# Kernel optimization log

Hardware: AMD Instinct MI355X
Metric: run time of the kernel (lower is better)

The kernel has to match this reference:

```python
import jax, jax.numpy as jnp
import numpy as np

# ---- module hyperparameters (from init_kwargs) ----
R, C = 16, 16            # layer.rows, layer.cols
STRIDE = 0               # layer.stride (shared receptive field)
KH = KW = 8              # layer.kernel_size
CIN, COUT = 16, 64       # in/out channels
T = 7                    # spike time steps (== maxweight)
MAXW = 7.0
UCAPTURE, UMINUS, USEARCH, UBACKOFF, UMIN = 0.102, 0.051, 0.032, 0.96, 0.008


def setup_inputs() -> dict:
    key = jax.random.key(0)
    k1, k2, k3 = jax.random.split(key, 3)
    input_spikes = jax.random.randint(k1, (T, CIN, KH, KW), 0, 2).astype(jnp.int32)
    output_spikes = jax.random.randint(k2, (T, COUT, R, C), 0, 2).astype(jnp.int32)
    # integer-valued weights in [0, maxweight], stored as float for the update math
    weight = jax.random.randint(k3, (R, C, COUT, CIN, KH, KW), 0, int(MAXW) + 1).astype(jnp.float32)
    return {"weight": weight, "input_spikes": input_spikes, "output_spikes": output_spikes}


def reference(weight, input_spikes, output_spikes):
    # spike-time codes: fewer spikes -> later time
    x_times = int(MAXW) - jnp.sum(input_spikes, axis=0)    # [CIN, KH, KW] (H==KH, W==KW)
    y_times = int(MAXW) - jnp.sum(output_spikes, axis=0)   # [COUT, R, C]

    # gather the receptive-field patch for every (row, col) column (static indices)
    rr = (np.arange(R) * STRIDE)[:, None] + np.arange(KH)  # [R, KH]
    cc = (np.arange(C) * STRIDE)[:, None] + np.arange(KW)  # [C, KW]
    # advanced indexing -> [CIN, R, C, KH, KW]
    x_patch = x_times[:, rr[:, None, :, None], cc[None, :, None, :]]
    bx = jnp.transpose(x_patch, (1, 2, 0, 3, 4))[:, :, None, :, :, :]   # [R,C,1,CIN,KH,KW]
    by = jnp.transpose(y_times, (1, 2, 0))[:, :, :, None, None, None]   # [R,C,COUT,1,1,1]

    A = bx == int(MAXW)
    B = by == int(MAXW)
    Cgt = bx > by

    zero = jnp.float32(0.0)
    probs_plus = jnp.where(~A & B, USEARCH, jnp.where(~A & ~B & ~Cgt, UCAPTURE, zero))
    probs_minus = jnp.where(A & ~B, UBACKOFF, jnp.where(~A & ~B & Cgt, UMINUS, zero))
    # broadcast to full weight shape
    shape = weight.shape
    probs_plus = jnp.broadcast_to(probs_plus, shape)
    probs_minus = jnp.broadcast_to(probs_minus, shape)

    key = jax.random.key(42)
    k1, k2, k3, k4, k5 = jax.random.split(key, 5)
    dt = weight.dtype
    bern_plus = (jax.random.uniform(k1, shape) < probs_plus)
    bern_minus = (jax.random.uniform(k2, shape) < probs_minus)

    ratio = weight * (1.0 / MAXW)
    F_minus_raw = jax.random.uniform(k3, shape) < (1.0 - ratio) * (1.0 + ratio)
    F_plus_raw = jax.random.uniform(k4, shape) < ratio * (2.0 - ratio)
    umin_bern = jax.random.uniform(k5, shape) < UMIN
    # torch.max of two {0,1} frames == logical OR
    F_plus = jnp.logical_or(F_plus_raw, umin_bern).astype(dt)
    F_minus = jnp.logical_or(F_minus_raw, umin_bern).astype(dt)

    new_w = weight + bern_plus.astype(dt) * F_plus - bern_minus.astype(dt) * F_minus
    new_w = jnp.clip(new_w, 0.0, MAXW)  # integer-valued floats, cast to int in torch
    return new_w
```

## Files before the change

### kernel.cpp

```cpp
#include <hip/hip_runtime.h>
#include <stdint.h>


#define N_TOTAL 16777216
#define Y_SIZE 16384
#define X_SIZE 1024

struct U2 { uint32_t a, b; };

constexpr uint32_t rotl_c(uint32_t x, int r) {
  return (x << r) | (x >> (32 - r));
}

constexpr U2 threefry_c(uint32_t k0, uint32_t k1, uint32_t x0, uint32_t x1) {
  uint32_t ks2 = k0 ^ k1 ^ 0x1BD11BDAu;
  x0 += k0; x1 += k1;
  x0 += x1; x1 = rotl_c(x1, 13); x1 ^= x0;
  x0 += x1; x1 = rotl_c(x1, 15); x1 ^= x0;
  x0 += x1; x1 = rotl_c(x1, 26); x1 ^= x0;
  x0 += x1; x1 = rotl_c(x1, 6);  x1 ^= x0;
  x0 += k1; x1 += ks2 + 1u;
  x0 += x1; x1 = rotl_c(x1, 17); x1 ^= x0;
  x0 += x1; x1 = rotl_c(x1, 29); x1 ^= x0;
  x0 += x1; x1 = rotl_c(x1, 16); x1 ^= x0;
  x0 += x1; x1 = rotl_c(x1, 24); x1 ^= x0;
  x0 += ks2; x1 += k0 + 2u;
  x0 += x1; x1 = rotl_c(x1, 13); x1 ^= x0;
  x0 += x1; x1 = rotl_c(x1, 15); x1 ^= x0;
  x0 += x1; x1 = rotl_c(x1, 26); x1 ^= x0;
  x0 += x1; x1 = rotl_c(x1, 6);  x1 ^= x0;
  x0 += k0; x1 += k1 + 3u;
  x0 += x1; x1 = rotl_c(x1, 17); x1 ^= x0;
  x0 += x1; x1 = rotl_c(x1, 29); x1 ^= x0;
  x0 += x1; x1 = rotl_c(x1, 16); x1 ^= x0;
  x0 += x1; x1 = rotl_c(x1, 24); x1 ^= x0;
  x0 += k1; x1 += ks2 + 4u;
  x0 += x1; x1 = rotl_c(x1, 13); x1 ^= x0;
  x0 += x1; x1 = rotl_c(x1, 15); x1 ^= x0;
  x0 += x1; x1 = rotl_c(x1, 26); x1 ^= x0;
  x0 += x1; x1 = rotl_c(x1, 6);  x1 ^= x0;
  x0 += ks2; x1 += k0 + 5u;
  return {x0, x1};
}

constexpr U2 SK1 = threefry_c(0u, 42u, 0u, 0u);
constexpr U2 SK2 = threefry_c(0u, 42u, 0u, 1u);
constexpr U2 SK3 = threefry_c(0u, 42u, 0u, 2u);
constexpr U2 SK4 = threefry_c(0u, 42u, 0u, 3u);
constexpr U2 SK5 = threefry_c(0u, 42u, 0u, 4u);

constexpr uint32_t KS2_3 = SK3.a ^ SK3.b ^ 0x1BD11BDAu;
constexpr uint32_t KS2_4 = SK4.a ^ SK4.b ^ 0x1BD11BDAu;
constexpr uint32_t KS2_5 = SK5.a ^ SK5.b ^ 0x1BD11BDAu;

constexpr uint32_t bern_thr(float pf) {
  double p8 = (double)pf * 8388608.0;
  uint64_t t = (uint64_t)p8;
  if ((double)t < p8) t += 1u;
  return (uint32_t)(t << 9);
}
constexpr uint32_t T_SEARCH  = bern_thr(0.032f);
constexpr uint32_t T_CAPTURE = bern_thr(0.102f);
constexpr uint32_t T_BACKOFF = bern_thr(0.96f);
constexpr uint32_t T_MINUS   = bern_thr(0.051f);
constexpr uint32_t T_UMIN    = bern_thr(0.008f);

__device__ __forceinline__ uint32_t rotl_d(uint32_t x, int r) {
  return __builtin_amdgcn_alignbit(x, x, 32 - r);
}

__device__ __forceinline__ uint32_t tf_fold_k(uint32_t k0, uint32_t k1,
                                              uint32_t ks2, uint32_t ctr) {
  uint32_t x0 = k0;
  uint32_t x1 = ctr + k1;
  x0 += x1; x1 = rotl_d(x1, 13); x1 ^= x0;
  x0 += x1; x1 = rotl_d(x1, 15); x1 ^= x0;
  x0 += x1; x1 = rotl_d(x1, 26); x1 ^= x0;
  x0 += x1; x1 = rotl_d(x1, 6);  x1 ^= x0;
  x0 += k1; x1 += ks2 + 1u;
  x0 += x1; x1 = rotl_d(x1, 17); x1 ^= x0;
  x0 += x1; x1 = rotl_d(x1, 29); x1 ^= x0;
  x0 += x1; x1 = rotl_d(x1, 16); x1 ^= x0;
  x0 += x1; x1 = rotl_d(x1, 24); x1 ^= x0;
  x0 += ks2; x1 += k0 + 2u;
  x0 += x1; x1 = rotl_d(x1, 13); x1 ^= x0;
  x0 += x1; x1 = rotl_d(x1, 15); x1 ^= x0;
  x0 += x1; x1 = rotl_d(x1, 26); x1 ^= x0;
  x0 += x1; x1 = rotl_d(x1, 6);  x1 ^= x0;
  x0 += k0; x1 += k1 + 3u;
  x0 += x1; x1 = rotl_d(x1, 17); x1 ^= x0;
  x0 += x1; x1 = rotl_d(x1, 29); x1 ^= x0;
  x0 += x1; x1 = rotl_d(x1, 16); x1 ^= x0;
  x0 += x1; x1 = rotl_d(x1, 24); x1 ^= x0;
  x0 += k1; x1 += ks2 + 4u;
  x0 += x1; x1 = rotl_d(x1, 13); x1 ^= x0;
  x0 += x1; x1 = rotl_d(x1, 15); x1 ^= x0;
  x0 += x1; x1 = rotl_d(x1, 26); x1 ^= x0;
  x0 += x1; x1 = rotl_d(x1, 6);  x1 ^= x0;
  x0 += ks2; x1 += k0 + 5u;
  return x0 ^ x1;
}

__device__ __forceinline__ float bits_to_unit_float(uint32_t bits) {
  uint32_t fb = (bits >> 9) | 0x3f800000u;
  return __uint_as_float(fb) - 1.0f;
}

__device__ __forceinline__ uint32_t mbcnt64(uint64_t m) {
  return __builtin_amdgcn_mbcnt_hi((uint32_t)(m >> 32),
         __builtin_amdgcn_mbcnt_lo((uint32_t)m, 0u));
}

__global__ void precompute_times(const int* __restrict__ in_sp,
                                 const int* __restrict__ out_sp,
                                 int* __restrict__ xt, int* __restrict__ yt) {
  int tid = blockIdx.x * 256 + threadIdx.x;
  if (tid < Y_SIZE) {
    int s = 0;
#pragma unroll
    for (int t = 0; t < 7; ++t) s += out_sp[t * Y_SIZE + tid];
    yt[tid] = 7 - s;
  } else if (tid < Y_SIZE + X_SIZE) {
    int j = tid - Y_SIZE;
    int s = 0;
#pragma unroll
    for (int t = 0; t < 7; ++t) s += in_sp[t * X_SIZE + j];
    xt[j] = 7 - s;
  }
}

__global__ __launch_bounds__(256) void modstdp4t(const float* __restrict__ w,
                                                 const int* __restrict__ xt,
                                                 const int* __restrict__ yt,
                                                 float* __restrict__ out) {
  __shared__ uint4 tbl[64];
  __shared__ uint2 rec[1024];
  __shared__ uint32_t okb[1024];

  uint32_t tid = threadIdx.x;

  if (tid < 64u) {
    uint32_t bx = tid >> 3, by = tid & 7u;
    bool A = (bx == 7u), B = (by == 7u), Cg = (bx > by);
    uint32_t thr = A ? (B ? 0u : T_BACKOFF)
                     : (B ? T_SEARCH : (Cg ? T_MINUS : T_CAPTURE));
    bool selM = A ? !B : (!B && Cg);
    uint32_t k0 = selM ? SK2.a : SK1.a;
    uint32_t k1 = selM ? SK2.b : SK1.b;
    tbl[tid] = make_uint4(thr | (uint32_t)selM, k0, k1,
                          k0 ^ k1 ^ 0x1BD11BDAu);
  }
  __syncthreads();

  uint32_t lane = tid & 63u;
  uint32_t wbase = (tid >> 6) * 256u;
  uint32_t t = blockIdx.x * 256u + tid;
  uint32_t i0 = t * 4u;

  float4 wv = *reinterpret_cast<const float4*>(w + i0);
  int4 bxv = *reinterpret_cast<const int4*>(xt + (i0 & 1023u));
  float warr[4]; *reinterpret_cast<float4*>(warr) = wv;
  int barr[4];   *reinterpret_cast<int4*>(barr) = bxv;

  uint32_t cout = (i0 >> 10) & 63u;
  uint32_t c = (i0 >> 16) & 15u;
  uint32_t r = i0 >> 20;
  uint32_t by = (uint32_t)yt[cout * 256u + r * 16u + c];

  bool hit[4];
  uint32_t sMb[4];
  uint32_t rank[4];
  uint32_t cnt = 0;

#pragma unroll
  for (int e = 0; e < 4; ++e) {
    uint32_t i = i0 + (uint32_t)e;
    uint4 en = tbl[(uint32_t)barr[e] * 8u + by];
    uint32_t thr = en.x & 0xFFFFFE00u;
    uint32_t selMb = en.x & 1u;
    sMb[e] = selMb;

    uint32_t bits12 = tf_fold_k(en.y, en.z, en.w, i);
    bool h = bits12 < thr;
    hit[e] = h;

    uint64_t m = __ballot(h);
    cnt += (uint32_t)__popcll(m);
    if (h) {
      uint32_t rk = (cnt - (uint32_t)__popcll(m)) + mbcnt64(m);
      rank[e] = rk;
      rec[wbase + rk] = make_uint2(i | (selMb << 31),
                                   __float_as_uint(warr[e]));
    }
  }

  for (uint32_t base = 0; base < cnt; base += 64u) {
    uint32_t idx = base + lane;
    if (idx < cnt) {
      uint2 rc = rec[wbase + idx];
      bool sm = (rc.x >> 31) != 0u;
      uint32_t ctr = rc.x & 0x7fffffffu;
      float wf = __uint_as_float(rc.y);

      const float inv7 = (float)(1.0 / 7.0);
      float ratio = __fmul_rn(wf, inv7);
      float thrF = sm
          ? __fmul_rn(__fsub_rn(1.0f, ratio), __fadd_rn(1.0f, ratio))
          : __fmul_rn(ratio, __fsub_rn(2.0f, ratio));

      uint32_t k34a = sm ? SK3.a : SK4.a;
      uint32_t k34b = sm ? SK3.b : SK4.b;
      uint32_t ks34 = sm ? KS2_3 : KS2_4;
      uint32_t bits34 = tf_fold_k(k34a, k34b, ks34, ctr);
      uint32_t bits5 = tf_fold_k(SK5.a, SK5.b, KS2_5, ctr);
      bool ok = (bits_to_unit_float(bits34) < thrF) | (bits5 < T_UMIN);
      okb[wbase + idx] = ok ? 1u : 0u;
    }
  }

  float res[4];
#pragma unroll
  for (int e = 0; e < 4; ++e) {
    float d = 0.0f;
    if (hit[e]) {
      uint32_t ok = okb[wbase + rank[e]];
      d = ok ? (sMb[e] ? -1.0f : 1.0f) : 0.0f;
    }
    res[e] = __builtin_amdgcn_fmed3f(warr[e] + d, 0.0f, 7.0f);
  }
  *reinterpret_cast<float4*>(out + i0) =
      make_float4(res[0], res[1], res[2], res[3]);
}

extern "C" void kernel_launch(void* const* d_in, const int* in_sizes, int n_in,
                              void* d_out, int out_size, void* d_ws, size_t ws_size,
                              hipStream_t stream) {
  const float* w = (const float*)d_in[0];
  const int* isp = (const int*)d_in[1];
  const int* osp = (const int*)d_in[2];
  float* out = (float*)d_out;
  int* xt = (int*)d_ws;
  int* yt = ((int*)d_ws) + X_SIZE;

  precompute_times<<<(Y_SIZE + X_SIZE + 255) / 256, 256, 0, stream>>>(isp, osp, xt, yt);
  modstdp4t<<<N_TOTAL / 4 / 256, 256, 0, stream>>>(w, xt, yt, out);
}
```

Measured before the change: 64.35 us.

## Process eight elements per thread with ballot-mask results and inline threshold logic

```diff
diff --git a/kernel.cpp b/kernel.cpp
--- a/kernel.cpp
+++ b/kernel.cpp
@@ -49,6 +49,8 @@
 constexpr U2 SK4 = threefry_c(0u, 42u, 0u, 3u);
 constexpr U2 SK5 = threefry_c(0u, 42u, 0u, 4u);
 
+constexpr uint32_t KS2_1 = SK1.a ^ SK1.b ^ 0x1BD11BDAu;
+constexpr uint32_t KS2_2 = SK2.a ^ SK2.b ^ 0x1BD11BDAu;
 constexpr uint32_t KS2_3 = SK3.a ^ SK3.b ^ 0x1BD11BDAu;
 constexpr uint32_t KS2_4 = SK4.a ^ SK4.b ^ 0x1BD11BDAu;
 constexpr uint32_t KS2_5 = SK5.a ^ SK5.b ^ 0x1BD11BDAu;
@@ -111,6 +113,23 @@
          __builtin_amdgcn_mbcnt_lo((uint32_t)m, 0u));
 }
 
+__device__ __forceinline__ bool helper_ok(uint2 rc) {
+  bool sm = (rc.x >> 31) != 0u;
+  uint32_t ctr = rc.x & 0x7fffffffu;
+  float wf = __uint_as_float(rc.y);
+  const float inv7 = (float)(1.0 / 7.0);
+  float ratio = __fmul_rn(wf, inv7);
+  float thrF = sm
+      ? __fmul_rn(__fsub_rn(1.0f, ratio), __fadd_rn(1.0f, ratio))
+      : __fmul_rn(ratio, __fsub_rn(2.0f, ratio));
+  uint32_t k0 = sm ? SK3.a : SK4.a;
+  uint32_t k1 = sm ? SK3.b : SK4.b;
+  uint32_t ks = sm ? KS2_3 : KS2_4;
+  uint32_t b34 = tf_fold_k(k0, k1, ks, ctr);
+  uint32_t b5 = tf_fold_k(SK5.a, SK5.b, KS2_5, ctr);
+  return (bits_to_unit_float(b34) < thrF) | (b5 < T_UMIN);
+}
+
 __global__ void precompute_times(const int* __restrict__ in_sp,
                                  const int* __restrict__ out_sp,
                                  int* __restrict__ xt, int* __restrict__ yt) {
@@ -129,107 +148,107 @@
   }
 }
 
-__global__ __launch_bounds__(256) void modstdp4t(const float* __restrict__ w,
-                                                 const int* __restrict__ xt,
-                                                 const int* __restrict__ yt,
-                                                 float* __restrict__ out) {
-  __shared__ uint4 tbl[64];
-  __shared__ uint2 rec[1024];
-  __shared__ uint32_t okb[1024];
+__global__ __launch_bounds__(256) void modstdp8(const float* __restrict__ w,
+                                                const int* __restrict__ xt,
+                                                const int* __restrict__ yt,
+                                                float* __restrict__ out) {
+  __shared__ uint2 rec[4 * 512];
+  __shared__ uint64_t okm[4 * 8];
 
   uint32_t tid = threadIdx.x;
-
-  if (tid < 64u) {
-    uint32_t bx = tid >> 3, by = tid & 7u;
-    bool A = (bx == 7u), B = (by == 7u), Cg = (bx > by);
-    uint32_t thr = A ? (B ? 0u : T_BACKOFF)
-                     : (B ? T_SEARCH : (Cg ? T_MINUS : T_CAPTURE));
-    bool selM = A ? !B : (!B && Cg);
-    uint32_t k0 = selM ? SK2.a : SK1.a;
-    uint32_t k1 = selM ? SK2.b : SK1.b;
-    tbl[tid] = make_uint4(thr | (uint32_t)selM, k0, k1,
-                          k0 ^ k1 ^ 0x1BD11BDAu);
-  }
-  __syncthreads();
-
   uint32_t lane = tid & 63u;
-  uint32_t wbase = (tid >> 6) * 256u;
+  uint32_t ws = tid >> 6;
   uint32_t t = blockIdx.x * 256u + tid;
-  uint32_t i0 = t * 4u;
-
-  float4 wv = *reinterpret_cast<const float4*>(w + i0);
-  int4 bxv = *reinterpret_cast<const int4*>(xt + (i0 & 1023u));
-  float warr[4]; *reinterpret_cast<float4*>(warr) = wv;
-  int barr[4];   *reinterpret_cast<int4*>(barr) = bxv;
+  uint32_t i0 = t * 8u;
+
+  float4 wa = *reinterpret_cast<const float4*>(w + i0);
+  float4 wb = *reinterpret_cast<const float4*>(w + i0 + 4u);
+  int4 xa = *reinterpret_cast<const int4*>(xt + (i0 & 1023u));
+  int4 xb = *reinterpret_cast<const int4*>(xt + (i0 & 1023u) + 4u);
+  float warr[8];
+  *reinterpret_cast<float4*>(warr) = wa;
+  *reinterpret_cast<float4*>(warr + 4) = wb;
+  int barr[8];
+  *reinterpret_cast<int4*>(barr) = xa;
+  *reinterpret_cast<int4*>(barr + 4) = xb;
 
   uint32_t cout = (i0 >> 10) & 63u;
   uint32_t c = (i0 >> 16) & 15u;
   uint32_t r = i0 >> 20;
-  uint32_t by = (uint32_t)yt[cout * 256u + r * 16u + c];
-
-  bool hit[4];
-  uint32_t sMb[4];
-  uint32_t rank[4];
+  int by = yt[cout * 256u + r * 16u + c];
+  bool B = (by == 7);
+  int mb6 = min(by, 6);
+
+  bool hit[8], sM[8];
+  uint32_t rank[8];
   uint32_t cnt = 0;
 
 #pragma unroll
-  for (int e = 0; e < 4; ++e) {
+  for (int e = 0; e < 8; ++e) {
     uint32_t i = i0 + (uint32_t)e;
-    uint4 en = tbl[(uint32_t)barr[e] * 8u + by];
-    uint32_t thr = en.x & 0xFFFFFE00u;
-    uint32_t selMb = en.x & 1u;
-    sMb[e] = selMb;
-
-    uint32_t bits12 = tf_fold_k(en.y, en.z, en.w, i);
+    int bx = barr[e];
+    bool A = (bx == 7);
+    bool selm = (!B) && (bx > mb6);
+    sM[e] = selm;
+    uint32_t thr = selm ? (A ? T_BACKOFF : T_MINUS)
+                        : (B ? (A ? 0u : T_SEARCH) : T_CAPTURE);
+    uint32_t k0 = selm ? SK2.a : SK1.a;
+    uint32_t k1 = selm ? SK2.b : SK1.b;
+    uint32_t ks = selm ? KS2_2 : KS2_1;
+    uint32_t bits12 = tf_fold_k(k0, k1, ks, i);
     bool h = bits12 < thr;
     hit[e] = h;
 
     uint64_t m = __ballot(h);
+    uint32_t rk = 0;
+    if (h) {
+      rk = cnt + mbcnt64(m);
+      rec[ws * 512u + rk] = make_uint2(i | (selm ? 0x80000000u : 0u),
+                                       __float_as_uint(warr[e]));
+    }
+    rank[e] = rk;
     cnt += (uint32_t)__popcll(m);
-    if (h) {
-      uint32_t rk = (cnt - (uint32_t)__popcll(m)) + mbcnt64(m);
-      rank[e] = rk;
-      rec[wbase + rk] = make_uint2(i | (selMb << 31),
-                                   __float_as_uint(warr[e]));
-    }
-  }
-
-  for (uint32_t base = 0; base < cnt; base += 64u) {
-    uint32_t idx = base + lane;
-    if (idx < cnt) {
-      uint2 rc = rec[wbase + idx];
-      bool sm = (rc.x >> 31) != 0u;
-      uint32_t ctr = rc.x & 0x7fffffffu;
-      float wf = __uint_as_float(rc.y);
-
-      const float inv7 = (float)(1.0 / 7.0);
-      float ratio = __fmul_rn(wf, inv7);
-      float thrF = sm
-          ? __fmul_rn(__fsub_rn(1.0f, ratio), __fadd_rn(1.0f, ratio))
-          : __fmul_rn(ratio, __fsub_rn(2.0f, ratio));
-
-      uint32_t k34a = sm ? SK3.a : SK4.a;
-      uint32_t k34b = sm ? SK3.b : SK4.b;
-      uint32_t ks34 = sm ? KS2_3 : KS2_4;
-      uint32_t bits34 = tf_fold_k(k34a, k34b, ks34, ctr);
-      uint32_t bits5 = tf_fold_k(SK5.a, SK5.b, KS2_5, ctr);
-      bool ok = (bits_to_unit_float(bits34) < thrF) | (bits5 < T_UMIN);
-      okb[wbase + idx] = ok ? 1u : 0u;
-    }
-  }
-
-  float res[4];
-#pragma unroll
-  for (int e = 0; e < 4; ++e) {
-    float d = 0.0f;
-    if (hit[e]) {
-      uint32_t ok = okb[wbase + rank[e]];
-      d = ok ? (sMb[e] ? -1.0f : 1.0f) : 0.0f;
-    }
-    res[e] = __builtin_amdgcn_fmed3f(warr[e] + d, 0.0f, 7.0f);
-  }
-  *reinterpret_cast<float4*>(out + i0) =
-      make_float4(res[0], res[1], res[2], res[3]);
+  }
+
+  uint64_t okmask0;
+  {
+    bool ok = false;
+    if (lane < cnt) ok = helper_ok(rec[ws * 512u + lane]);
+    okmask0 = __ballot(ok);
+  }
+
+  if (__builtin_expect(cnt > 64u, 0)) {
+    if (lane == 0u) okm[ws * 8u] = okmask0;
+    for (uint32_t base = 64u; base < cnt; base += 64u) {
+      bool ok = false;
+      uint32_t idx = base + lane;
+      if (idx < cnt) ok = helper_ok(rec[ws * 512u + idx]);
+      uint64_t mm = __ballot(ok);
+      if (lane == 0u) okm[ws * 8u + (base >> 6)] = mm;
+    }
+    float res[8];
+#pragma unroll
+    for (int e = 0; e < 8; ++e) {
+      uint64_t mask = okm[ws * 8u + (rank[e] >> 6)];
+      uint32_t ob = (uint32_t)(mask >> (rank[e] & 63u)) & 1u;
+      float d = (hit[e] && ob) ? (sM[e] ? -1.0f : 1.0f) : 0.0f;
+      res[e] = __builtin_amdgcn_fmed3f(warr[e] + d, 0.0f, 7.0f);
+    }
+    *reinterpret_cast<float4*>(out + i0) = *reinterpret_cast<float4*>(res);
+    *reinterpret_cast<float4*>(out + i0 + 4u) =
+        *reinterpret_cast<float4*>(res + 4);
+  } else {
+    float res[8];
+#pragma unroll
+    for (int e = 0; e < 8; ++e) {
+      uint32_t ob = (uint32_t)(okmask0 >> rank[e]) & 1u;
+      float d = (hit[e] && ob) ? (sM[e] ? -1.0f : 1.0f) : 0.0f;
+      res[e] = __builtin_amdgcn_fmed3f(warr[e] + d, 0.0f, 7.0f);
+    }
+    *reinterpret_cast<float4*>(out + i0) = *reinterpret_cast<float4*>(res);
+    *reinterpret_cast<float4*>(out + i0 + 4u) =
+        *reinterpret_cast<float4*>(res + 4);
+  }
 }
 
 extern "C" void kernel_launch(void* const* d_in, const int* in_sizes, int n_in,
@@ -243,5 +262,5 @@
   int* yt = ((int*)d_ws) + X_SIZE;
 
   precompute_times<<<(Y_SIZE + X_SIZE + 255) / 256, 256, 0, stream>>>(isp, osp, xt, yt);
-  modstdp4t<<<N_TOTAL / 4 / 256, 256, 0, stream>>>(w, xt, yt, out);
-}
+  modstdp8<<<N_TOTAL / 8 / 256, 256, 0, stream>>>(w, xt, yt, out);
+}
```

Measured after the change: 59.10 us. 1.09x faster.
